# Kernel tuning notes

Measured on AMD Instinct MI355X. Metric: run time of the kernel, lower is better.

The kernel has to match this reference:

```python
import jax, jax.numpy as jnp
import numpy as np

E = 8      # num_expert
D = 1024   # d_model
H = 2048   # expert hidden (htoh4 size)
K = 2      # top_k
N = 2048   # tokens (batch*seq)


def setup_inputs() -> dict:
    key = jax.random.key(0)
    ks = jax.random.split(key, 4)
    sc = lambda k, shape, s: jax.random.normal(k, shape, jnp.float32) * s
    return {
        "inp": jax.random.normal(ks[0], (N, D), jnp.float32),
        "Wg": sc(ks[1], (D, E), D ** -0.5),          # NaiveGate linear
        "bg": jnp.zeros((E,), jnp.float32),
        "W1": sc(ks[2], (E, D, H), D ** -0.5),        # per-expert htoh4
        "b1": jnp.zeros((E, H), jnp.float32),
        "W2": sc(ks[3], (E, H, D), H ** -0.5),        # per-expert h4toh
        "b2": jnp.zeros((E, D), jnp.float32),
    }


def reference(inp, Wg, bg, W1, b1, W2, b2):
    # NaiveGate: linear -> top_k logits -> softmax over the k selected logits
    logits = inp @ Wg + bg                              # [N, E]
    top_val, top_idx = jax.lax.top_k(logits, K)         # [N, K]
    gate_score = jax.nn.softmax(top_val, axis=-1)       # [N, K]

    # Expert grouped compute. Reference computes every expert on every token
    # (exact math, no capacity dropping); combine selects the routed ones.
    h = jax.nn.gelu(jnp.einsum('nd,edh->neh', inp, W1) + b1)   # [N, E, H]
    y = jnp.einsum('neh,ehd->ned', h, W2) + b2                 # [N, E, D]

    # Combine: equivalent to bmm(gate_score[N,1,K], x[N,K,D]) after gather.
    comb = jnp.sum(jax.nn.one_hot(top_idx, E, dtype=inp.dtype)
                   * gate_score[..., None], axis=1)            # [N, E]
    return jnp.einsum('ne,ned->nd', comb, y)                   # [N, D]
```

## Files before the change

kernel.cpp:

```cpp
#include <hip/hip_runtime.h>
#include <math.h>

#define N_TOK 2048
#define DM    1024
#define HD    2048
#define NE    8
#define RMAX  5120
#define TMAX  40
#define KSPL  2

#define GATE_BLKS 512
#define XCVT_BLKS 1024
#define WCV1_BLKS 2048
#define PREP_BLKS (GATE_BLKS + XCVT_BLKS + WCV1_BLKS)
#define FFN1_BLKS (8 * 4 * TMAX)
#define WCV2_BLKS 2048

typedef short short8 __attribute__((ext_vector_type(8)));
typedef unsigned short u16x8 __attribute__((ext_vector_type(8)));
typedef float f32x4  __attribute__((ext_vector_type(4)));

__device__ inline unsigned short f2b(float f) {
  unsigned int u = __float_as_uint(f);
  return (unsigned short)((u + 0x7FFFu + ((u >> 16) & 1u)) >> 16);
}
__device__ inline float b2f(unsigned short s) {
  return __uint_as_float(((unsigned int)s) << 16);
}
__device__ inline void gload_lds16(const void* g, void* l) {
  __builtin_amdgcn_global_load_lds(
      (const __attribute__((address_space(1))) unsigned int*)g,
      (__attribute__((address_space(3))) unsigned int*)l, 16, 0, 0);
}

__device__ inline void wcvt_tile(const float* __restrict__ src,
                                 unsigned short* __restrict__ dst,
                                 int N, int n0, int k0, int tid) {
  int cg = tid & 63, kg = tid >> 6;
  const float* s = src + (size_t)(k0 + kg * 8) * N + n0 + cg * 4;
  float4 v[8];
#pragma unroll
  for (int i = 0; i < 8; ++i) v[i] = *(const float4*)(s + (size_t)i * N);
#pragma unroll
  for (int c = 0; c < 4; ++c) {
    u16x8 o;
    o[0] = f2b(v[0][c]); o[1] = f2b(v[1][c]); o[2] = f2b(v[2][c]); o[3] = f2b(v[3][c]);
    o[4] = f2b(v[4][c]); o[5] = f2b(v[5][c]); o[6] = f2b(v[6][c]); o[7] = f2b(v[7][c]);
    *(u16x8*)(dst + ((size_t)(k0 / 8 + kg) * N + n0 + cg * 4 + c) * 8) = o;
  }
}

__global__ __launch_bounds__(256) void prep_kernel(
    const float* __restrict__ inp, const float* __restrict__ Wg,
    const float* __restrict__ bg,  const float* __restrict__ W1,
    int* __restrict__ top_idx, float* __restrict__ gate_w,
    unsigned short* __restrict__ Xb, unsigned short* __restrict__ W1C) {
  int bid = blockIdx.x;
  if (bid < GATE_BLKS) {
    int wave = threadIdx.x >> 6;
    int lane = threadIdx.x & 63;
    int n = bid * 4 + wave;
    float acc[NE];
#pragma unroll
    for (int e = 0; e < NE; ++e) acc[e] = 0.f;
    const float4* wg4 = reinterpret_cast<const float4*>(Wg);
#pragma unroll
    for (int i = 0; i < DM / 64; ++i) {
      int d = i * 64 + lane;
      float x = inp[n * DM + d];
      float4 w0 = wg4[d * 2 + 0];
      float4 w1 = wg4[d * 2 + 1];
      acc[0] += x * w0.x; acc[1] += x * w0.y; acc[2] += x * w0.z; acc[3] += x * w0.w;
      acc[4] += x * w1.x; acc[5] += x * w1.y; acc[6] += x * w1.z; acc[7] += x * w1.w;
    }
#pragma unroll
    for (int off = 32; off > 0; off >>= 1) {
#pragma unroll
      for (int e = 0; e < NE; ++e) acc[e] += __shfl_xor(acc[e], off);
    }
    if (lane == 0) {
      float v0 = -1e30f, v1 = -1e30f; int i0 = -1, i1 = -1;
#pragma unroll
      for (int e = 0; e < NE; ++e) {
        float v = acc[e] + bg[e];
        if (v > v0)      { v1 = v0; i1 = i0; v0 = v; i0 = e; }
        else if (v > v1) { v1 = v;  i1 = e; }
      }
      float e1 = expf(v1 - v0);
      float s  = 1.f + e1;
      top_idx[n * 2]     = i0;
      top_idx[n * 2 + 1] = i1;
      gate_w[n * 2]      = 1.f / s;
      gate_w[n * 2 + 1]  = e1 / s;
    }
  } else if (bid < GATE_BLKS + XCVT_BLKS) {
    int i = ((bid - GATE_BLKS) * 256 + threadIdx.x) * 8;
    float4 a = *(const float4*)(inp + i);
    float4 b = *(const float4*)(inp + i + 4);
    ushort4 pa, pb;
    pa.x = f2b(a.x); pa.y = f2b(a.y); pa.z = f2b(a.z); pa.w = f2b(a.w);
    pb.x = f2b(b.x); pb.y = f2b(b.y); pb.z = f2b(b.z); pb.w = f2b(b.w);
    *(ushort4*)(Xb + i)     = pa;
    *(ushort4*)(Xb + i + 4) = pb;
  } else {
    int wb = bid - (GATE_BLKS + XCVT_BLKS);
    int z  = wb >> 8;
    int r  = wb & 255;
    int gx = r & 7, gy = r >> 3;
    wcvt_tile(W1 + (size_t)z * DM * HD, W1C + (size_t)z * DM * HD,
              HD, gx * 256, gy * 32, threadIdx.x);
  }
}

__global__ __launch_bounds__(1024) void group_kernel(
    const int* __restrict__ top_idx,
    int* __restrict__ token_of, int* __restrict__ inv_g,
    int* __restrict__ tile_expert, int* __restrict__ tile_row0,
    int* __restrict__ n_tiles) {
  __shared__ int s_wtot[16];
  int tid = threadIdx.x, lane = tid & 63, wid = tid >> 6;
  int base = 0, tiles = 0;
  for (int e = 0; e < NE; ++e) {
    int cnt = 0;
#pragma unroll
    for (int c0 = 0; c0 < N_TOK; c0 += 1024) {
      int n = c0 + tid;
      int t0 = top_idx[n * 2], t1 = top_idx[n * 2 + 1];
      bool f = (t0 == e) || (t1 == e);
      int k = (t0 == e) ? 0 : 1;
      unsigned long long m = __ballot(f);
      int lp = __popcll(m & ((1ull << lane) - 1ull));
      if (lane == 0) s_wtot[wid] = __popcll(m);
      __syncthreads();
      int wbase = 0, tot = 0;
#pragma unroll
      for (int w = 0; w < 16; ++w) {
        int c = s_wtot[w];
        if (w < wid) wbase += c;
        tot += c;
      }
      if (f) {
        int pos = base + cnt + wbase + lp;
        token_of[pos] = n;
        inv_g[n * 2 + k] = pos;
      }
      cnt += tot;
      __syncthreads();
    }
    int padded = (cnt + 127) & ~127;
    for (int i = cnt + tid; i < padded; i += 1024) token_of[base + i] = -1;
    if (tid == 0) {
      for (int t = 0; t < padded / 128; ++t) {
        tile_expert[tiles + t] = e;
        tile_row0[tiles + t]   = base + t * 128;
      }
    }
    tiles += padded / 128;
    base  += padded;
    __syncthreads();
  }
  if (tid == 0) n_tiles[0] = tiles;
}

__global__ __launch_bounds__(256, 6) void ffn1_mfma(
    const unsigned short* __restrict__ Xb,
    const unsigned short* __restrict__ W1C,
    const float* __restrict__ b1,
    const unsigned short* __restrict__ Xzero,
    const int* __restrict__ token_of, const int* __restrict__ tile_expert,
    const int* __restrict__ tile_row0, const int* __restrict__ n_tiles,
    unsigned short* __restrict__ Hbuf,
    const float* __restrict__ W2, unsigned short* __restrict__ W2C) {
  int bid = blockIdx.x;
  if (bid >= FFN1_BLKS) {
    int wb = bid - FFN1_BLKS;
    int z  = wb >> 8;
    int r  = wb & 255;
    int gx = r & 3, gy = r >> 2;
    wcvt_tile(W2 + (size_t)z * HD * DM, W2C + (size_t)z * HD * DM,
              DM, gx * 256, gy * 32, threadIdx.x);
    return;
  }
  int xcd  = bid & 7, slot = bid >> 3;
  int unit = xcd * 4 + slot / TMAX;
  int t    = slot % TMAX;
  if (t >= n_tiles[0]) return;
  int e    = tile_expert[t];
  int row0 = tile_row0[t];
  int h0   = unit * 64;
  __shared__ __align__(16) unsigned short Asl[2][128][32];
  __shared__ __align__(16) unsigned short Bsl[2][4][64][8];
  int tid = threadIdx.x, lane = tid & 63;
  int wid = tid >> 6, wr = wid >> 1, wc = wid & 1;
  int l15 = lane & 15, l4 = lane >> 4;
  int sw  = (l15 >> 1) & 3;

  int ar[2], asg[2], tk[2];
#pragma unroll
  for (int q = 0; q < 2; ++q) {
    int idx = tid + q * 256;
    ar[q]  = idx >> 2;
    asg[q] = (idx & 3) ^ ((ar[q] >> 1) & 3);
    tk[q]  = token_of[row0 + ar[q]];
  }
  int bcol = tid & 63, bks = tid >> 6;
  const unsigned short* W1e = W1C + (size_t)e * DM * HD;

  f32x4 acc[4][2] = {};

  auto issueAB = [&](int tt, int buf) {
#pragma unroll
    for (int q = 0; q < 2; ++q) {
      int idx = tid + q * 256;
      const unsigned short* ga = (tk[q] < 0)
          ? Xzero
          : Xb + (size_t)tk[q] * DM + tt * 32 + asg[q] * 8;
      gload_lds16(ga, (char*)&Asl[buf][0][0] + (size_t)idx * 16);
    }
    const unsigned short* gb =
        W1e + ((size_t)(tt * 4 + bks) * HD + h0 + bcol) * 8;
    gload_lds16(gb, (char*)&Bsl[buf][0][0] + (size_t)tid * 16);
  };
  auto compute = [&](int buf) {
    short8 a[4], b[2];
#pragma unroll
    for (int m = 0; m < 4; ++m) {
      int R = wr * 64 + m * 16 + l15;
      a[m] = *(const short8*)((const char*)&Asl[buf][0][0] + R * 64 + ((l4 ^ sw) << 4));
    }
#pragma unroll
    for (int n = 0; n < 2; ++n)
      b[n] = *(const short8*)&Bsl[buf][l4][wc * 32 + n * 16 + l15][0];
#pragma unroll
    for (int m = 0; m < 4; ++m)
#pragma unroll
      for (int n = 0; n < 2; ++n)
        acc[m][n] = __builtin_amdgcn_mfma_f32_16x16x32_bf16(a[m], b[n], acc[m][n], 0, 0, 0);
  };

  issueAB(0, 0);
  for (int kt = 0; kt < 32; kt += 2) {
    __syncthreads();
    if (kt + 1 < 32) issueAB(kt + 1, 1);
    compute(0);
    __syncthreads();
    if (kt + 2 < 32) issueAB(kt + 2, 0);
    compute(1);
  }

  float bias[2];
#pragma unroll
  for (int n = 0; n < 2; ++n) bias[n] = b1[e * HD + h0 + wc * 32 + n * 16 + l15];
#pragma unroll
  for (int m = 0; m < 4; ++m) {
#pragma unroll
    for (int n = 0; n < 2; ++n) {
      int col = h0 + wc * 32 + n * 16 + l15;
#pragma unroll
      for (int j = 0; j < 4; ++j) {
        int row = row0 + wr * 64 + m * 16 + l4 * 4 + j;
        float x = acc[m][n][j] + bias[n];
        float g = 0.5f * x * (1.f + tanhf(0.7978845608f * (x + 0.044715f * x * x * x)));
        Hbuf[(size_t)row * HD + col] = f2b(g);
      }
    }
  }
}

__global__ __launch_bounds__(256, 6) void ffn2_mfma(
    const unsigned short* __restrict__ Hbuf,
    const unsigned short* __restrict__ W2C,
    const float* __restrict__ b2,
    const int* __restrict__ tile_expert, const int* __restrict__ tile_row0,
    const int* __restrict__ n_tiles,
    float* __restrict__ Ypart) {
  int lin  = blockIdx.x;
  int xcd  = lin & 7, slot = lin >> 3;
  int unit = xcd * 4 + slot / TMAX;
  int t    = slot % TMAX;
  if (t >= n_tiles[0]) return;
  int e    = tile_expert[t];
  int row0 = tile_row0[t];
  int d0   = (unit >> 1) * 64;
  int ks   = unit & 1;
  int kbase = ks * (HD / KSPL);
  int kb0   = kbase >> 3;
  __shared__ __align__(16) unsigned short Asl[2][128][32];
  __shared__ __align__(16) unsigned short Bsl[2][4][64][8];
  int tid = threadIdx.x, lane = tid & 63;
  int wid = tid >> 6, wr = wid >> 1, wc = wid & 1;
  int l15 = lane & 15, l4 = lane >> 4;
  int sw  = (l15 >> 1) & 3;

  int ar[2], asg[2];
#pragma unroll
  for (int q = 0; q < 2; ++q) {
    int idx = tid + q * 256;
    ar[q]  = idx >> 2;
    asg[q] = (idx & 3) ^ ((ar[q] >> 1) & 3);
  }
  int bcol = tid & 63, bks = tid >> 6;
  const unsigned short* W2e = W2C + (size_t)e * HD * DM;

  f32x4 acc[4][2] = {};

  auto issueAB = [&](int tt, int buf) {
#pragma unroll
    for (int q = 0; q < 2; ++q) {
      int idx = tid + q * 256;
      const unsigned short* ga =
          Hbuf + (size_t)(row0 + ar[q]) * HD + kbase + tt * 32 + asg[q] * 8;
      gload_lds16(ga, (char*)&Asl[buf][0][0] + (size_t)idx * 16);
    }
    const unsigned short* gb =
        W2e + ((size_t)(kb0 + tt * 4 + bks) * DM + d0 + bcol) * 8;
    gload_lds16(gb, (char*)&Bsl[buf][0][0] + (size_t)tid * 16);
  };
  auto compute = [&](int buf) {
    short8 a[4], b[2];
#pragma unroll
    for (int m = 0; m < 4; ++m) {
      int R = wr * 64 + m * 16 + l15;
      a[m] = *(const short8*)((const char*)&Asl[buf][0][0] + R * 64 + ((l4 ^ sw) << 4));
    }
#pragma unroll
    for (int n = 0; n < 2; ++n)
      b[n] = *(const short8*)&Bsl[buf][l4][wc * 32 + n * 16 + l15][0];
#pragma unroll
    for (int m = 0; m < 4; ++m)
#pragma unroll
      for (int n = 0; n < 2; ++n)
        acc[m][n] = __builtin_amdgcn_mfma_f32_16x16x32_bf16(a[m], b[n], acc[m][n], 0, 0, 0);
  };

  const int NT = HD / KSPL / 32;
  issueAB(0, 0);
  for (int kt = 0; kt < NT; kt += 2) {
    __syncthreads();
    if (kt + 1 < NT) issueAB(kt + 1, 1);
    compute(0);
    __syncthreads();
    if (kt + 2 < NT) issueAB(kt + 2, 0);
    compute(1);
  }

  float bias[2];
#pragma unroll
  for (int n = 0; n < 2; ++n)
    bias[n] = (ks == 0) ? b2[e * DM + d0 + wc * 32 + n * 16 + l15] : 0.f;
  float* Yp = Ypart + (size_t)ks * RMAX * DM;
#pragma unroll
  for (int m = 0; m < 4; ++m) {
#pragma unroll
    for (int n = 0; n < 2; ++n) {
      int col = d0 + wc * 32 + n * 16 + l15;
#pragma unroll
      for (int j = 0; j < 4; ++j) {
        int row = row0 + wr * 64 + m * 16 + l4 * 4 + j;
        Yp[(size_t)row * DM + col] = acc[m][n][j] + bias[n];
      }
    }
  }
}

__global__ void combine_kernel(const float* __restrict__ Ypart,
                               const int* __restrict__ inv_g,
                               const float* __restrict__ gate_w,
                               float* __restrict__ out) {
  int n = blockIdx.x;
  int r0 = inv_g[n * 2], r1 = inv_g[n * 2 + 1];
  float g0 = gate_w[n * 2], g1 = gate_w[n * 2 + 1];
  int i = threadIdx.x;
  const float4* y00 = (const float4*)(Ypart + (size_t)r0 * DM);
  const float4* y01 = (const float4*)(Ypart + (size_t)(RMAX + r0) * DM);
  const float4* y10 = (const float4*)(Ypart + (size_t)r1 * DM);
  const float4* y11 = (const float4*)(Ypart + (size_t)(RMAX + r1) * DM);
  float4 a0 = y00[i], a1 = y01[i], b0 = y10[i], b1 = y11[i];
  float4 rv;
  rv.x = g0 * (a0.x + a1.x) + g1 * (b0.x + b1.x);
  rv.y = g0 * (a0.y + a1.y) + g1 * (b0.y + b1.y);
  rv.z = g0 * (a0.z + a1.z) + g1 * (b0.z + b1.z);
  rv.w = g0 * (a0.w + a1.w) + g1 * (b0.w + b1.w);
  *(float4*)(out + (size_t)n * DM + i * 4) = rv;
}

extern "C" void kernel_launch(void* const* d_in, const int* in_sizes, int n_in,
                              void* d_out, int out_size, void* d_ws, size_t ws_size,
                              hipStream_t stream) {
  const float* inp = (const float*)d_in[0];
  const float* Wg  = (const float*)d_in[1];
  const float* bg  = (const float*)d_in[2];
  const float* W1  = (const float*)d_in[3];
  const float* b1  = (const float*)d_in[4];
  const float* W2  = (const float*)d_in[5];
  const float* b2  = (const float*)d_in[6];
  float* out = (float*)d_out;

  char* ws = (char*)d_ws;
  size_t off = 0;
  auto alloc = [&](size_t bytes) {
    size_t o = off;
    off = (off + bytes + 255) & ~(size_t)255;
    return o;
  };
  int*   top_idx     = (int*)  (ws + alloc(N_TOK * 2 * sizeof(int)));
  float* gate_w      = (float*)(ws + alloc(N_TOK * 2 * sizeof(float)));
  int*   token_of    = (int*)  (ws + alloc(RMAX * sizeof(int)));
  int*   inv_g       = (int*)  (ws + alloc(N_TOK * 2 * sizeof(int)));
  int*   tile_expert = (int*)  (ws + alloc(TMAX * sizeof(int)));
  int*   tile_row0   = (int*)  (ws + alloc(TMAX * sizeof(int)));
  int*   n_tiles     = (int*)  (ws + alloc(sizeof(int)));
  unsigned short* Xzero = (unsigned short*)(ws + alloc(DM * 2));
  unsigned short* Xb    = (unsigned short*)(ws + alloc((size_t)N_TOK * DM * 2));
  unsigned short* W1C   = (unsigned short*)(ws + alloc((size_t)NE * DM * HD * 2));
  unsigned short* W2C   = (unsigned short*)(ws + alloc((size_t)NE * HD * DM * 2));
  unsigned short* Hbuf  = (unsigned short*)(ws + alloc((size_t)RMAX * HD * 2));
  float*          Ypart = (float*)(ws + alloc((size_t)KSPL * RMAX * DM * 4));
  (void)ws_size;

  hipMemsetAsync(Xzero, 0, DM * 2, stream);
  prep_kernel<<<PREP_BLKS, 256, 0, stream>>>(inp, Wg, bg, W1,
                                             top_idx, gate_w, Xb, W1C);
  group_kernel<<<1, 1024, 0, stream>>>(top_idx, token_of, inv_g,
                                       tile_expert, tile_row0, n_tiles);
  ffn1_mfma<<<FFN1_BLKS + WCV2_BLKS, 256, 0, stream>>>(
      Xb, W1C, b1, Xzero, token_of, tile_expert, tile_row0, n_tiles, Hbuf,
      W2, W2C);
  ffn2_mfma<<<8 * 4 * TMAX, 256, 0, stream>>>(
      Hbuf, W2C, b2, tile_expert, tile_row0, n_tiles, Ypart);
  combine_kernel<<<N_TOK, 256, 0, stream>>>(Ypart, inv_g, gate_w, out);
}
```

Measured before the change: 157.2 us.

## Triple-buffer MFMA GEMM pipelines and move W2 conversion into prep kernel

Both expert GEMM kernels move from a double-buffered loop with two __syncthreads per pair of k-steps to a three-stage ring buffer. Each step waits with s_waitcnt vmcnt(3) and uses a single barrier, so two tiles of loads stay in flight while one is computed. The W2 fp32-to-bf16 conversion moves out of the ffn1 launch into prep_kernel, so ffn1 no longer shares the GPU with conversion blocks. In exchange, LDS use per block grows by half and the occupancy hint drops from 6 to 4 blocks. The new vmcnt-based synchronization also relies on the exact count of outstanding loads per issue.

Result: slower. 164.9 us (+4.9%).

```diff
diff --git a/kernel.cpp b/kernel.cpp
--- a/kernel.cpp
+++ b/kernel.cpp
@@ -12,9 +12,8 @@
 #define GATE_BLKS 512
 #define XCVT_BLKS 1024
 #define WCV1_BLKS 2048
-#define PREP_BLKS (GATE_BLKS + XCVT_BLKS + WCV1_BLKS)
-#define FFN1_BLKS (8 * 4 * TMAX)
 #define WCV2_BLKS 2048
+#define PREP_BLKS (GATE_BLKS + XCVT_BLKS + WCV1_BLKS + WCV2_BLKS)
 
 typedef short short8 __attribute__((ext_vector_type(8)));
 typedef unsigned short u16x8 __attribute__((ext_vector_type(8)));
@@ -53,8 +52,10 @@
 __global__ __launch_bounds__(256) void prep_kernel(
     const float* __restrict__ inp, const float* __restrict__ Wg,
     const float* __restrict__ bg,  const float* __restrict__ W1,
+    const float* __restrict__ W2,
     int* __restrict__ top_idx, float* __restrict__ gate_w,
-    unsigned short* __restrict__ Xb, unsigned short* __restrict__ W1C) {
+    unsigned short* __restrict__ Xb,
+    unsigned short* __restrict__ W1C, unsigned short* __restrict__ W2C) {
   int bid = blockIdx.x;
   if (bid < GATE_BLKS) {
     int wave = threadIdx.x >> 6;
@@ -102,13 +103,20 @@
     pb.x = f2b(b.x); pb.y = f2b(b.y); pb.z = f2b(b.z); pb.w = f2b(b.w);
     *(ushort4*)(Xb + i)     = pa;
     *(ushort4*)(Xb + i + 4) = pb;
-  } else {
+  } else if (bid < GATE_BLKS + XCVT_BLKS + WCV1_BLKS) {
     int wb = bid - (GATE_BLKS + XCVT_BLKS);
     int z  = wb >> 8;
     int r  = wb & 255;
     int gx = r & 7, gy = r >> 3;
     wcvt_tile(W1 + (size_t)z * DM * HD, W1C + (size_t)z * DM * HD,
               HD, gx * 256, gy * 32, threadIdx.x);
+  } else {
+    int wb = bid - (GATE_BLKS + XCVT_BLKS + WCV1_BLKS);
+    int z  = wb >> 8;
+    int r  = wb & 255;
+    int gx = r & 3, gy = r >> 2;
+    wcvt_tile(W2 + (size_t)z * HD * DM, W2C + (size_t)z * HD * DM,
+              DM, gx * 256, gy * 32, threadIdx.x);
   }
 }
 
@@ -162,34 +170,24 @@
   if (tid == 0) n_tiles[0] = tiles;
 }
 
-__global__ __launch_bounds__(256, 6) void ffn1_mfma(
+__global__ __launch_bounds__(256, 4) void ffn1_mfma(
     const unsigned short* __restrict__ Xb,
     const unsigned short* __restrict__ W1C,
     const float* __restrict__ b1,
     const unsigned short* __restrict__ Xzero,
     const int* __restrict__ token_of, const int* __restrict__ tile_expert,
     const int* __restrict__ tile_row0, const int* __restrict__ n_tiles,
-    unsigned short* __restrict__ Hbuf,
-    const float* __restrict__ W2, unsigned short* __restrict__ W2C) {
-  int bid = blockIdx.x;
-  if (bid >= FFN1_BLKS) {
-    int wb = bid - FFN1_BLKS;
-    int z  = wb >> 8;
-    int r  = wb & 255;
-    int gx = r & 3, gy = r >> 2;
-    wcvt_tile(W2 + (size_t)z * HD * DM, W2C + (size_t)z * HD * DM,
-              DM, gx * 256, gy * 32, threadIdx.x);
-    return;
-  }
-  int xcd  = bid & 7, slot = bid >> 3;
+    unsigned short* __restrict__ Hbuf) {
+  int lin  = blockIdx.x;
+  int xcd  = lin & 7, slot = lin >> 3;
   int unit = xcd * 4 + slot / TMAX;
   int t    = slot % TMAX;
   if (t >= n_tiles[0]) return;
   int e    = tile_expert[t];
   int row0 = tile_row0[t];
   int h0   = unit * 64;
-  __shared__ __align__(16) unsigned short Asl[2][128][32];
-  __shared__ __align__(16) unsigned short Bsl[2][4][64][8];
+  __shared__ __align__(16) unsigned short Asl[3][128][32];
+  __shared__ __align__(16) unsigned short Bsl[3][4][64][8];
   int tid = threadIdx.x, lane = tid & 63;
   int wid = tid >> 6, wr = wid >> 1, wc = wid & 1;
   int l15 = lane & 15, l4 = lane >> 4;
@@ -239,14 +237,23 @@
   };
 
   issueAB(0, 0);
-  for (int kt = 0; kt < 32; kt += 2) {
-    __syncthreads();
-    if (kt + 1 < 32) issueAB(kt + 1, 1);
-    compute(0);
-    __syncthreads();
-    if (kt + 2 < 32) issueAB(kt + 2, 0);
-    compute(1);
-  }
+  issueAB(1, 1);
+  int buf = 0;
+  for (int kt = 0; kt < 31; ++kt) {
+    asm volatile("s_waitcnt vmcnt(3)" ::: "memory");
+    __builtin_amdgcn_s_barrier();
+    __builtin_amdgcn_sched_barrier(0);
+    compute(buf);
+    if (kt + 2 < 32) {
+      int nb = buf + 2; if (nb >= 3) nb -= 3;
+      issueAB(kt + 2, nb);
+    }
+    if (++buf == 3) buf = 0;
+  }
+  asm volatile("s_waitcnt vmcnt(0)" ::: "memory");
+  __builtin_amdgcn_s_barrier();
+  __builtin_amdgcn_sched_barrier(0);
+  compute(buf);
 
   float bias[2];
 #pragma unroll
@@ -267,7 +274,7 @@
   }
 }
 
-__global__ __launch_bounds__(256, 6) void ffn2_mfma(
+__global__ __launch_bounds__(256, 4) void ffn2_mfma(
     const unsigned short* __restrict__ Hbuf,
     const unsigned short* __restrict__ W2C,
     const float* __restrict__ b2,
@@ -285,8 +292,8 @@
   int ks   = unit & 1;
   int kbase = ks * (HD / KSPL);
   int kb0   = kbase >> 3;
-  __shared__ __align__(16) unsigned short Asl[2][128][32];
-  __shared__ __align__(16) unsigned short Bsl[2][4][64][8];
+  __shared__ __align__(16) unsigned short Asl[3][128][32];
+  __shared__ __align__(16) unsigned short Bsl[3][4][64][8];
   int tid = threadIdx.x, lane = tid & 63;
   int wid = tid >> 6, wr = wid >> 1, wc = wid & 1;
   int l15 = lane & 15, l4 = lane >> 4;
@@ -335,14 +342,23 @@
 
   const int NT = HD / KSPL / 32;
   issueAB(0, 0);
-  for (int kt = 0; kt < NT; kt += 2) {
-    __syncthreads();
-    if (kt + 1 < NT) issueAB(kt + 1, 1);
-    compute(0);
-    __syncthreads();
-    if (kt + 2 < NT) issueAB(kt + 2, 0);
-    compute(1);
-  }
+  issueAB(1, 1);
+  int buf = 0;
+  for (int kt = 0; kt < NT - 1; ++kt) {
+    asm volatile("s_waitcnt vmcnt(3)" ::: "memory");
+    __builtin_amdgcn_s_barrier();
+    __builtin_amdgcn_sched_barrier(0);
+    compute(buf);
+    if (kt + 2 < NT) {
+      int nb = buf + 2; if (nb >= 3) nb -= 3;
+      issueAB(kt + 2, nb);
+    }
+    if (++buf == 3) buf = 0;
+  }
+  asm volatile("s_waitcnt vmcnt(0)" ::: "memory");
+  __builtin_amdgcn_s_barrier();
+  __builtin_amdgcn_sched_barrier(0);
+  compute(buf);
 
   float bias[2];
 #pragma unroll
@@ -419,13 +435,12 @@
   (void)ws_size;
 
   hipMemsetAsync(Xzero, 0, DM * 2, stream);
-  prep_kernel<<<PREP_BLKS, 256, 0, stream>>>(inp, Wg, bg, W1,
-                                             top_idx, gate_w, Xb, W1C);
+  prep_kernel<<<PREP_BLKS, 256, 0, stream>>>(inp, Wg, bg, W1, W2,
+                                             top_idx, gate_w, Xb, W1C, W2C);
   group_kernel<<<1, 1024, 0, stream>>>(top_idx, token_of, inv_g,
                                        tile_expert, tile_row0, n_tiles);
-  ffn1_mfma<<<FFN1_BLKS + WCV2_BLKS, 256, 0, stream>>>(
-      Xb, W1C, b1, Xzero, token_of, tile_expert, tile_row0, n_tiles, Hbuf,
-      W2, W2C);
+  ffn1_mfma<<<8 * 4 * TMAX, 256, 0, stream>>>(
+      Xb, W1C, b1, Xzero, token_of, tile_expert, tile_row0, n_tiles, Hbuf);
   ffn2_mfma<<<8 * 4 * TMAX, 256, 0, stream>>>(
       Hbuf, W2C, b2, tile_expert, tile_row0, n_tiles, Ypart);
   combine_kernel<<<N_TOK, 256, 0, stream>>>(Ypart, inv_g, gate_w, out);
```
